# Kernel tuning notes

Measured on AMD Instinct MI355X. Metric: run time of the kernel, lower is better.

Reference implementation:

```python
import jax, jax.numpy as jnp
import numpy as np

NDIM = 2
NSIG = 2
NCELLS = 1000
BATCH = 4
DT = 1e-3
NSTEPS = 251  # 1 + int((t1 - t0)/dt) with t0=0, t1=0.25
SIGMA = 1e-3


def _phi(y, pw1, pb1, pw2, pb2, pw3, pb3, pw4, pb4, pw5, pb5):
    # phi_nn: 2 -> 16 -> 32 -> 32 -> 16 -> 1 with tanh activations
    h = jnp.tanh(y @ pw1.T + pb1)
    h = jnp.tanh(h @ pw2.T + pb2)
    h = jnp.tanh(h @ pw3.T + pb3)
    h = jnp.tanh(h @ pw4.T + pb4)
    return h @ pw5.T + pb5  # (ncells, 1)


def setup_inputs() -> dict:
    key = jax.random.key(0)
    ks = jax.random.split(key, 16)
    # x = [t0, t1, y0.flat, tcrit, p0(2), p1(2)] per batch item
    y0 = 0.1 * jax.random.normal(ks[0], (BATCH, NCELLS, NDIM), dtype=jnp.float32)
    t0 = jnp.zeros((BATCH, 1), jnp.float32)
    t1 = jnp.full((BATCH, 1), 0.25, jnp.float32)
    tcrit = jnp.full((BATCH, 1), 0.125, jnp.float32)
    p0 = jax.random.normal(ks[1], (BATCH, 2), dtype=jnp.float32)
    p1 = jax.random.normal(ks[2], (BATCH, 2), dtype=jnp.float32)
    x = jnp.concatenate([t0, t1, y0.reshape(BATCH, -1), tcrit, p0, p1], axis=1)
    # Wiener increments ~ N(0, dt)
    dw = np.sqrt(DT).astype(np.float32) * jax.random.normal(
        ks[3], (BATCH, NSTEPS, NCELLS, NDIM), dtype=jnp.float32)
    # phi_nn weights (torch Linear: weight is (out, in)), init N(0, 0.1), bias 0
    def w(k, o, i):
        return 0.1 * jax.random.normal(k, (o, i), dtype=jnp.float32)
    inp = dict(x=x, dw=dw,
               pw1=w(ks[4], 16, 2), pb1=jnp.zeros(16, jnp.float32),
               pw2=w(ks[5], 32, 16), pb2=jnp.zeros(32, jnp.float32),
               pw3=w(ks[6], 32, 32), pb3=jnp.zeros(32, jnp.float32),
               pw4=w(ks[7], 16, 32), pb4=jnp.zeros(16, jnp.float32),
               pw5=w(ks[8], 1, 16), pb5=jnp.zeros(1, jnp.float32),
               tw=w(ks[9], NDIM, NSIG), tb=jnp.zeros(NDIM, jnp.float32))
    return inp


def reference(x, dw, pw1, pb1, pw2, pb2, pw3, pb3, pw4, pb4, pw5, pb5, tw, tb):
    phi_params = (pw1, pb1, pw2, pb2, pw3, pb3, pw4, pb4, pw5, pb5)
    grad_phi = jax.grad(lambda yy: jnp.sum(_phi(yy, *phi_params)))

    def simulate(xi, dwi):
        t0 = xi[0]
        y0 = xi[2:2 + NCELLS * NDIM].reshape(NCELLS, NDIM)
        ps = xi[2 + NCELLS * NDIM:]
        tcrit, p0, p1 = ps[0], ps[1:3], ps[3:5]
        ts = t0 + DT * jnp.arange(NSTEPS, dtype=xi.dtype)

        def step(y, t_dw):
            t, dwt = t_dw
            sig = jnp.where(t < tcrit, p0, p1)      # step signal f_signal(t, params)
            tilt = sig @ tw.T + tb                  # grad_tilt: (ndim,)
            drift = -(grad_phi(y) + tilt)           # f(t, y)
            y_new = y + drift * DT + SIGMA * dwt    # Euler-Maruyama
            return y_new, None

        y_final, _ = jax.lax.scan(step, y0, (ts, dwi))
        return y_final

    return jax.vmap(simulate)(x, dw)  # (BATCH, NCELLS, NDIM)
```

## Files before the change

### kernel.cpp

```cpp
#include <hip/hip_runtime.h>

#define NDIMC 2
#define NCELLS 1000
#define BATCHSZ 4
#define NSTEPS 251
#define XROW 2007

typedef float v2f __attribute__((ext_vector_type(2)));
typedef float v4f __attribute__((ext_vector_type(4)));

__device__ __forceinline__ v2f vlo(v4f v) { return __builtin_shufflevector(v, v, 0, 1); }
__device__ __forceinline__ v2f vhi(v4f v) { return __builtin_shufflevector(v, v, 2, 3); }

__device__ __forceinline__ v2f pfma(v2f w, v2f v, v2f a) {
    return __builtin_elementwise_fma(w, v, a);
}

__device__ __forceinline__ float fast_tanh(float x) {
    float e = __builtin_amdgcn_exp2f(x * 2.885390081777926774f);
    float r = __builtin_amdgcn_rcpf(e + 1.0f);
    return fmaf(-2.0f, r, 1.0f);
}


template<int CTRL>
__device__ __forceinline__ float dpp_add(float z) {
    int t = __builtin_amdgcn_update_dpp(0, __float_as_int(z), CTRL, 0xf, 0xf, true);
    return z + __int_as_float(t);
}
__device__ __forceinline__ float row16_sum(float z) {
    z = dpp_add<0xB1>(z);
    z = dpp_add<0x1B>(z);
    z = dpp_add<0x141>(z);
    z = dpp_add<0x140>(z);
    return z;
}

__device__ __forceinline__ float pdot16(const v2f (&w)[8], const float* p, float bias) {
    v4f u0 = *(const v4f*)(p);
    v4f u1 = *(const v4f*)(p + 4);
    v4f u2 = *(const v4f*)(p + 8);
    v4f u3 = *(const v4f*)(p + 12);
    v2f a0 = {bias, 0.f}, a1 = {0.f, 0.f}, a2 = {0.f, 0.f}, a3 = {0.f, 0.f};
    a0 = pfma(w[0], vlo(u0), a0); a1 = pfma(w[1], vhi(u0), a1);
    a2 = pfma(w[2], vlo(u1), a2); a3 = pfma(w[3], vhi(u1), a3);
    a0 = pfma(w[4], vlo(u2), a0); a1 = pfma(w[5], vhi(u2), a1);
    a2 = pfma(w[6], vlo(u3), a2); a3 = pfma(w[7], vhi(u3), a3);
    v2f s = (a0 + a1) + (a2 + a3);
    return s[0] + s[1];
}

__device__ __forceinline__ float pdot32(const v2f (&w)[16], const float* p, float bias) {
    v2f a0 = {bias, 0.f}, a1 = {0.f, 0.f}, a2 = {0.f, 0.f}, a3 = {0.f, 0.f};
    #pragma unroll
    for (int c = 0; c < 2; ++c) {
        v4f u0 = *(const v4f*)(p + c * 16);
        v4f u1 = *(const v4f*)(p + c * 16 + 4);
        v4f u2 = *(const v4f*)(p + c * 16 + 8);
        v4f u3 = *(const v4f*)(p + c * 16 + 12);
        a0 = pfma(w[c*8+0], vlo(u0), a0); a1 = pfma(w[c*8+1], vhi(u0), a1);
        a2 = pfma(w[c*8+2], vlo(u1), a2); a3 = pfma(w[c*8+3], vhi(u1), a3);
        a0 = pfma(w[c*8+4], vlo(u2), a0); a1 = pfma(w[c*8+5], vhi(u2), a1);
        a2 = pfma(w[c*8+6], vlo(u3), a2); a3 = pfma(w[c*8+7], vhi(u3), a3);
    }
    v2f s = (a0 + a1) + (a2 + a3);
    return s[0] + s[1];
}

__global__ __launch_bounds__(64, 2)
void phinn_sde_kernel(const float* __restrict__ x,   const float* __restrict__ dw,
                      const float* __restrict__ pw1, const float* __restrict__ pb1,
                      const float* __restrict__ pw2, const float* __restrict__ pb2,
                      const float* __restrict__ pw3, const float* __restrict__ pb3,
                      const float* __restrict__ pw4, const float* __restrict__ pb4,
                      const float* __restrict__ pw5, const float* __restrict__ pb5,
                      const float* __restrict__ tw,  const float* __restrict__ tb,
                      float* __restrict__ out)
{
    __shared__ float sh[2][6][32];

    const int tid  = threadIdx.x;
    const int n    = tid & 31;
    const int grp  = tid >> 5;
    const int s16  = n & 15;
    const int b    = blockIdx.x / (NCELLS / 2);
    const int pair = blockIdx.x % (NCELLS / 2);
    const int cell = pair * 2 + grp;

    const float r1a = pw1[s16 * 2 + 0];
    const float r1b = pw1[s16 * 2 + 1];
    const float rb1 = pb1[s16];
    const float rb2 = pb2[n];
    const float rb3 = pb3[n];
    const float rb4 = pb4[s16];
    const float rw5 = pw5[s16];

    v2f w2p[8];
    #pragma unroll
    for (int j = 0; j < 8; ++j) w2p[j] = ((const v2f*)pw2)[n * 8 + j];

    v2f w3p[16];
    #pragma unroll
    for (int j = 0; j < 16; ++j) w3p[j] = ((const v2f*)pw3)[n * 16 + j];

    v2f w4p[16];
    #pragma unroll
    for (int j = 0; j < 16; ++j) w4p[j] = ((const v2f*)pw4)[s16 * 16 + j];

    v2f w4cp[8];
    #pragma unroll
    for (int j = 0; j < 8; ++j)
        w4cp[j] = v2f{pw4[(2*j) * 32 + n], pw4[(2*j+1) * 32 + n]};

    v2f w3cp[16];
    #pragma unroll
    for (int j = 0; j < 16; ++j)
        w3cp[j] = v2f{pw3[(2*j) * 32 + n], pw3[(2*j+1) * 32 + n]};

    v2f w2cp[16];
    #pragma unroll
    for (int j = 0; j < 16; ++j)
        w2cp[j] = v2f{pw2[(2*j) * 16 + s16], pw2[(2*j+1) * 16 + s16]};

    const float* xb = x + (size_t)b * XROW;
    const float t0v    = xb[0];
    const float tcritv = xb[2 + NCELLS * NDIMC];
    const float p0x = xb[2003], p0y = xb[2004];
    const float p1x = xb[2005], p1y = xb[2006];
    const float tA0 = fmaf(p0x, tw[0], fmaf(p0y, tw[1], tb[0]));
    const float tA1 = fmaf(p0x, tw[2], fmaf(p0y, tw[3], tb[1]));
    const float tB0 = fmaf(p1x, tw[0], fmaf(p1y, tw[1], tb[0]));
    const float tB1 = fmaf(p1x, tw[2], fmaf(p1y, tw[3], tb[1]));

    float y0 = xb[2 + cell * 2 + 0];
    float y1 = xb[2 + cell * 2 + 1];

    const float* dwb = dw + (size_t)b * NSTEPS * NCELLS * NDIMC
                          + (size_t)pair * 2 * NDIMC;
    int dwoff = grp * NDIMC;

    const float* l0 = &sh[grp][0][0];
    const float* l1 = &sh[grp][1][0];
    const float* l2 = &sh[grp][2][0];
    const float* l3 = &sh[grp][3][0];
    const float* l4 = &sh[grp][4][0];
    const float* l5 = &sh[grp][5][0];

    #pragma unroll 1
    for (int i = 0; i < NSTEPS; ++i) {
        const float2 dwv = *(const float2*)(dwb + dwoff);
        dwoff += NCELLS * NDIMC;
        const float t = t0v + 0.001f * (float)i;

        const float h1 = fast_tanh(fmaf(r1a, y0, fmaf(r1b, y1, rb1)));
        sh[grp][0][n] = h1;

        const float h2 = fast_tanh(pdot16(w2p, l0, rb2));
        sh[grp][1][n] = h2;

        const float h3 = fast_tanh(pdot32(w3p, l1, rb3));
        sh[grp][2][n] = h3;

        const float h4 = fast_tanh(pdot32(w4p, l2, rb4));

        const float g4p = rw5 * fmaf(-h4, h4, 1.0f);
        sh[grp][3][n] = g4p;

        const float g3p = pdot16(w4cp, l3, 0.f) * fmaf(-h3, h3, 1.0f);
        sh[grp][4][n] = g3p;

        const float g2p = pdot32(w3cp, l4, 0.f) * fmaf(-h2, h2, 1.0f);
        sh[grp][5][n] = g2p;

        const float g1p = pdot32(w2cp, l5, 0.f) * fmaf(-h1, h1, 1.0f);

        const float v0 = row16_sum(r1a * g1p);
        const float v1 = row16_sum(r1b * g1p);

        const bool  cnd   = t < tcritv;
        const float tilt0 = cnd ? tA0 : tB0;
        const float tilt1 = cnd ? tA1 : tB1;
        y0 = fmaf(-0.001f, v0 + tilt0, fmaf(0.001f, dwv.x, y0));
        y1 = fmaf(-0.001f, v1 + tilt1, fmaf(0.001f, dwv.y, y1));
    }

    if (n == 0) {
        *(float2*)(out + ((size_t)b * NCELLS + cell) * NDIMC) = make_float2(y0, y1);
    }
}

extern "C" void kernel_launch(void* const* d_in, const int* in_sizes, int n_in,
                              void* d_out, int out_size, void* d_ws, size_t ws_size,
                              hipStream_t stream) {
    const float* x   = (const float*)d_in[0];
    const float* dw  = (const float*)d_in[1];
    const float* pw1 = (const float*)d_in[2];
    const float* pb1 = (const float*)d_in[3];
    const float* pw2 = (const float*)d_in[4];
    const float* pb2 = (const float*)d_in[5];
    const float* pw3 = (const float*)d_in[6];
    const float* pb3 = (const float*)d_in[7];
    const float* pw4 = (const float*)d_in[8];
    const float* pb4 = (const float*)d_in[9];
    const float* pw5 = (const float*)d_in[10];
    const float* pb5 = (const float*)d_in[11];
    const float* tw  = (const float*)d_in[12];
    const float* tb  = (const float*)d_in[13];
    float* out = (float*)d_out;

    dim3 grid(BATCHSZ * NCELLS / 2);
    dim3 block(64);
    phinn_sde_kernel<<<grid, block, 0, stream>>>(x, dw, pw1, pb1, pw2, pb2,
                                                 pw3, pb3, pw4, pb4, pw5, pb5,
                                                 tw, tb, out);
}
```

Measured before the change: 271.4 us.

## Split each cell's dot products across two wave halves with permlane16 swap reduction

Each 64-thread block now handles one cell instead of two. The two 16-lane halves of each 32-lane group each compute half of every dot product, and the partial sums are combined with v_permlane16_swap. This halves the per-thread weight registers and the serial FMA chain length per step, and doubles the grid with a higher occupancy target in the launch bounds. The cost is twice as many wavefronts, an extra cross-lane swap per layer, and more redundant LDS traffic.

```diff
diff --git a/kernel.cpp b/kernel.cpp
--- a/kernel.cpp
+++ b/kernel.cpp
@@ -36,12 +36,28 @@
     return z;
 }
 
-__device__ __forceinline__ float pdot16(const v2f (&w)[8], const float* p, float bias) {
+__device__ __forceinline__ float xor16(float z, bool odd) {
+    float t = z, u = z;
+    asm("v_permlane16_swap_b32 %0, %1" : "+v"(t), "+v"(u));
+    return odd ? t : u;
+}
+
+__device__ __forceinline__ float pdot8h(const v2f (&w)[4], const float* p) {
+    v4f u0 = *(const v4f*)(p);
+    v4f u1 = *(const v4f*)(p + 4);
+    v2f a0 = {0.f, 0.f}, a1 = {0.f, 0.f};
+    a0 = pfma(w[0], vlo(u0), a0); a1 = pfma(w[1], vhi(u0), a1);
+    a0 = pfma(w[2], vlo(u1), a0); a1 = pfma(w[3], vhi(u1), a1);
+    v2f s = a0 + a1;
+    return s[0] + s[1];
+}
+
+__device__ __forceinline__ float pdot16h(const v2f (&w)[8], const float* p) {
     v4f u0 = *(const v4f*)(p);
     v4f u1 = *(const v4f*)(p + 4);
     v4f u2 = *(const v4f*)(p + 8);
     v4f u3 = *(const v4f*)(p + 12);
-    v2f a0 = {bias, 0.f}, a1 = {0.f, 0.f}, a2 = {0.f, 0.f}, a3 = {0.f, 0.f};
+    v2f a0 = {0.f, 0.f}, a1 = {0.f, 0.f}, a2 = {0.f, 0.f}, a3 = {0.f, 0.f};
     a0 = pfma(w[0], vlo(u0), a0); a1 = pfma(w[1], vhi(u0), a1);
     a2 = pfma(w[2], vlo(u1), a2); a3 = pfma(w[3], vhi(u1), a3);
     a0 = pfma(w[4], vlo(u2), a0); a1 = pfma(w[5], vhi(u2), a1);
@@ -50,24 +66,7 @@
     return s[0] + s[1];
 }
 
-__device__ __forceinline__ float pdot32(const v2f (&w)[16], const float* p, float bias) {
-    v2f a0 = {bias, 0.f}, a1 = {0.f, 0.f}, a2 = {0.f, 0.f}, a3 = {0.f, 0.f};
-    #pragma unroll
-    for (int c = 0; c < 2; ++c) {
-        v4f u0 = *(const v4f*)(p + c * 16);
-        v4f u1 = *(const v4f*)(p + c * 16 + 4);
-        v4f u2 = *(const v4f*)(p + c * 16 + 8);
-        v4f u3 = *(const v4f*)(p + c * 16 + 12);
-        a0 = pfma(w[c*8+0], vlo(u0), a0); a1 = pfma(w[c*8+1], vhi(u0), a1);
-        a2 = pfma(w[c*8+2], vlo(u1), a2); a3 = pfma(w[c*8+3], vhi(u1), a3);
-        a0 = pfma(w[c*8+4], vlo(u2), a0); a1 = pfma(w[c*8+5], vhi(u2), a1);
-        a2 = pfma(w[c*8+6], vlo(u3), a2); a3 = pfma(w[c*8+7], vhi(u3), a3);
-    }
-    v2f s = (a0 + a1) + (a2 + a3);
-    return s[0] + s[1];
-}
-
-__global__ __launch_bounds__(64, 2)
+__global__ __launch_bounds__(64, 4)
 void phinn_sde_kernel(const float* __restrict__ x,   const float* __restrict__ dw,
                       const float* __restrict__ pw1, const float* __restrict__ pb1,
                       const float* __restrict__ pw2, const float* __restrict__ pb2,
@@ -77,15 +76,16 @@
                       const float* __restrict__ tw,  const float* __restrict__ tb,
                       float* __restrict__ out)
 {
-    __shared__ float sh[2][6][32];
+    __shared__ float sh[6][32];
 
     const int tid  = threadIdx.x;
-    const int n    = tid & 31;
-    const int grp  = tid >> 5;
-    const int s16  = n & 15;
-    const int b    = blockIdx.x / (NCELLS / 2);
-    const int pair = blockIdx.x % (NCELLS / 2);
-    const int cell = pair * 2 + grp;
+    const int s16  = tid & 15;
+    const int r    = tid >> 4;
+    const int kh   = r & 1;
+    const bool odd = kh;
+    const int n    = s16 + ((r >> 1) << 4);
+    const int b    = blockIdx.x / NCELLS;
+    const int cell = blockIdx.x % NCELLS;
 
     const float r1a = pw1[s16 * 2 + 0];
     const float r1b = pw1[s16 * 2 + 1];
@@ -95,32 +95,32 @@
     const float rb4 = pb4[s16];
     const float rw5 = pw5[s16];
 
-    v2f w2p[8];
-    #pragma unroll
-    for (int j = 0; j < 8; ++j) w2p[j] = ((const v2f*)pw2)[n * 8 + j];
-
-    v2f w3p[16];
-    #pragma unroll
-    for (int j = 0; j < 16; ++j) w3p[j] = ((const v2f*)pw3)[n * 16 + j];
-
-    v2f w4p[16];
-    #pragma unroll
-    for (int j = 0; j < 16; ++j) w4p[j] = ((const v2f*)pw4)[s16 * 16 + j];
-
-    v2f w4cp[8];
+    v2f w2p[4];
+    #pragma unroll
+    for (int j = 0; j < 4; ++j) w2p[j] = ((const v2f*)pw2)[n * 8 + kh * 4 + j];
+
+    v2f w3p[8];
+    #pragma unroll
+    for (int j = 0; j < 8; ++j) w3p[j] = ((const v2f*)pw3)[n * 16 + kh * 8 + j];
+
+    v2f w4p[8];
+    #pragma unroll
+    for (int j = 0; j < 8; ++j) w4p[j] = ((const v2f*)pw4)[s16 * 16 + kh * 8 + j];
+
+    v2f w4cp[4];
+    #pragma unroll
+    for (int j = 0; j < 4; ++j)
+        w4cp[j] = v2f{pw4[(kh*8 + 2*j) * 32 + n], pw4[(kh*8 + 2*j + 1) * 32 + n]};
+
+    v2f w3cp[8];
     #pragma unroll
     for (int j = 0; j < 8; ++j)
-        w4cp[j] = v2f{pw4[(2*j) * 32 + n], pw4[(2*j+1) * 32 + n]};
-
-    v2f w3cp[16];
-    #pragma unroll
-    for (int j = 0; j < 16; ++j)
-        w3cp[j] = v2f{pw3[(2*j) * 32 + n], pw3[(2*j+1) * 32 + n]};
-
-    v2f w2cp[16];
-    #pragma unroll
-    for (int j = 0; j < 16; ++j)
-        w2cp[j] = v2f{pw2[(2*j) * 16 + s16], pw2[(2*j+1) * 16 + s16]};
+        w3cp[j] = v2f{pw3[(kh*16 + 2*j) * 32 + n], pw3[(kh*16 + 2*j + 1) * 32 + n]};
+
+    v2f w2cp[8];
+    #pragma unroll
+    for (int j = 0; j < 8; ++j)
+        w2cp[j] = v2f{pw2[(kh*16 + 2*j) * 16 + s16], pw2[(kh*16 + 2*j + 1) * 16 + s16]};
 
     const float* xb = x + (size_t)b * XROW;
     const float t0v    = xb[0];
@@ -135,47 +135,51 @@
     float y0 = xb[2 + cell * 2 + 0];
     float y1 = xb[2 + cell * 2 + 1];
 
-    const float* dwb = dw + (size_t)b * NSTEPS * NCELLS * NDIMC
-                          + (size_t)pair * 2 * NDIMC;
-    int dwoff = grp * NDIMC;
-
-    const float* l0 = &sh[grp][0][0];
-    const float* l1 = &sh[grp][1][0];
-    const float* l2 = &sh[grp][2][0];
-    const float* l3 = &sh[grp][3][0];
-    const float* l4 = &sh[grp][4][0];
-    const float* l5 = &sh[grp][5][0];
+    const float* dwp = dw + ((size_t)b * NSTEPS * NCELLS + cell) * NDIMC;
+
+    const float* l0 = &sh[0][0];
+    const float* l1 = &sh[1][0];
+    const float* l2 = &sh[2][0];
+    const float* l3 = &sh[3][0];
+    const float* l4 = &sh[4][0];
+    const float* l5 = &sh[5][0];
 
     #pragma unroll 1
     for (int i = 0; i < NSTEPS; ++i) {
-        const float2 dwv = *(const float2*)(dwb + dwoff);
-        dwoff += NCELLS * NDIMC;
+        const float2 dwv = *(const float2*)dwp;
+        dwp += NCELLS * NDIMC;
         const float t = t0v + 0.001f * (float)i;
 
         const float h1 = fast_tanh(fmaf(r1a, y0, fmaf(r1b, y1, rb1)));
-        sh[grp][0][n] = h1;
-
-        const float h2 = fast_tanh(pdot16(w2p, l0, rb2));
-        sh[grp][1][n] = h2;
-
-        const float h3 = fast_tanh(pdot32(w3p, l1, rb3));
-        sh[grp][2][n] = h3;
-
-        const float h4 = fast_tanh(pdot32(w4p, l2, rb4));
-
-        const float g4p = rw5 * fmaf(-h4, h4, 1.0f);
-        sh[grp][3][n] = g4p;
-
-        const float g3p = pdot16(w4cp, l3, 0.f) * fmaf(-h3, h3, 1.0f);
-        sh[grp][4][n] = g3p;
-
-        const float g2p = pdot32(w3cp, l4, 0.f) * fmaf(-h2, h2, 1.0f);
-        sh[grp][5][n] = g2p;
-
-        const float g1p = pdot32(w2cp, l5, 0.f) * fmaf(-h1, h1, 1.0f);
-
-        const float v0 = row16_sum(r1a * g1p);
-        const float v1 = row16_sum(r1b * g1p);
+        sh[0][s16] = h1;
+
+        const float p2 = pdot8h(w2p, l0 + kh * 8);
+        const float h2 = fast_tanh(p2 + xor16(p2, odd) + rb2);
+        sh[1][n] = h2;
+
+        const float p3 = pdot16h(w3p, l1 + kh * 16);
+        const float h3 = fast_tanh(p3 + xor16(p3, odd) + rb3);
+        sh[2][n] = h3;
+
+        const float p4 = pdot16h(w4p, l2 + kh * 16);
+        const float h4 = fast_tanh(p4 + xor16(p4, odd) + rb4);
+
+        const float g4 = rw5 * fmaf(-h4, h4, 1.0f);
+        sh[3][s16] = g4;
+
+        const float q3 = pdot8h(w4cp, l3 + kh * 8);
+        const float g3 = (q3 + xor16(q3, odd)) * fmaf(-h3, h3, 1.0f);
+        sh[4][n] = g3;
+
+        const float q2 = pdot16h(w3cp, l4 + kh * 16);
+        const float g2 = (q2 + xor16(q2, odd)) * fmaf(-h2, h2, 1.0f);
+        sh[5][n] = g2;
+
+        const float q1 = pdot16h(w2cp, l5 + kh * 16);
+        const float g1 = (q1 + xor16(q1, odd)) * fmaf(-h1, h1, 1.0f);
+
+        const float v0 = row16_sum(r1a * g1);
+        const float v1 = row16_sum(r1b * g1);
 
         const bool  cnd   = t < tcritv;
         const float tilt0 = cnd ? tA0 : tB0;
@@ -184,7 +188,7 @@
         y1 = fmaf(-0.001f, v1 + tilt1, fmaf(0.001f, dwv.y, y1));
     }
 
-    if (n == 0) {
+    if (tid == 0) {
         *(float2*)(out + ((size_t)b * NCELLS + cell) * NDIMC) = make_float2(y0, y1);
     }
 }
@@ -208,7 +212,7 @@
     const float* tb  = (const float*)d_in[13];
     float* out = (float*)d_out;
 
-    dim3 grid(BATCHSZ * NCELLS / 2);
+    dim3 grid(BATCHSZ * NCELLS);
     dim3 block(64);
     phinn_sde_kernel<<<grid, block, 0, stream>>>(x, dw, pw1, pb1, pw2, pb2,
                                                  pw3, pb3, pw4, pb4, pw5, pb5,
```

Result: slower. 346.3 us (+27.6%).

## Replace reverse-mode gradient with forward-mode tangent propagation through the MLP

Applied to the files above, without the earlier changes.

Instead of a forward pass followed by a backward pass with transposed weights, the kernel now propagates two tangent vectors (one per input dimension) alongside activations in a single forward sweep. Each layer's dot products run three times on the same weights, and the transposed weight registers are dropped. This cuts the serial chain of layer stages and shared-memory round trips from seven to four, and frees registers. In exchange each layer does three times the dot-product work, which adds arithmetic and LDS reads per step.

```diff
diff --git a/kernel.cpp b/kernel.cpp
--- a/kernel.cpp
+++ b/kernel.cpp
@@ -77,7 +77,7 @@
                       const float* __restrict__ tw,  const float* __restrict__ tb,
                       float* __restrict__ out)
 {
-    __shared__ float sh[2][6][32];
+    __shared__ __align__(16) float sh[2][3][3][32];
 
     const int tid  = threadIdx.x;
     const int n    = tid & 31;
@@ -106,21 +106,6 @@
     v2f w4p[16];
     #pragma unroll
     for (int j = 0; j < 16; ++j) w4p[j] = ((const v2f*)pw4)[s16 * 16 + j];
-
-    v2f w4cp[8];
-    #pragma unroll
-    for (int j = 0; j < 8; ++j)
-        w4cp[j] = v2f{pw4[(2*j) * 32 + n], pw4[(2*j+1) * 32 + n]};
-
-    v2f w3cp[16];
-    #pragma unroll
-    for (int j = 0; j < 16; ++j)
-        w3cp[j] = v2f{pw3[(2*j) * 32 + n], pw3[(2*j+1) * 32 + n]};
-
-    v2f w2cp[16];
-    #pragma unroll
-    for (int j = 0; j < 16; ++j)
-        w2cp[j] = v2f{pw2[(2*j) * 16 + s16], pw2[(2*j+1) * 16 + s16]};
 
     const float* xb = x + (size_t)b * XROW;
     const float t0v    = xb[0];
@@ -139,12 +124,15 @@
                           + (size_t)pair * 2 * NDIMC;
     int dwoff = grp * NDIMC;
 
-    const float* l0 = &sh[grp][0][0];
-    const float* l1 = &sh[grp][1][0];
-    const float* l2 = &sh[grp][2][0];
-    const float* l3 = &sh[grp][3][0];
-    const float* l4 = &sh[grp][4][0];
-    const float* l5 = &sh[grp][5][0];
+    const float* L0h = &sh[grp][0][0][0];
+    const float* L0a = &sh[grp][0][1][0];
+    const float* L0b = &sh[grp][0][2][0];
+    const float* L1h = &sh[grp][1][0][0];
+    const float* L1a = &sh[grp][1][1][0];
+    const float* L1b = &sh[grp][1][2][0];
+    const float* L2h = &sh[grp][2][0][0];
+    const float* L2a = &sh[grp][2][1][0];
+    const float* L2b = &sh[grp][2][2][0];
 
     #pragma unroll 1
     for (int i = 0; i < NSTEPS; ++i) {
@@ -153,29 +141,37 @@
         const float t = t0v + 0.001f * (float)i;
 
         const float h1 = fast_tanh(fmaf(r1a, y0, fmaf(r1b, y1, rb1)));
-        sh[grp][0][n] = h1;
-
-        const float h2 = fast_tanh(pdot16(w2p, l0, rb2));
-        sh[grp][1][n] = h2;
-
-        const float h3 = fast_tanh(pdot32(w3p, l1, rb3));
-        sh[grp][2][n] = h3;
-
-        const float h4 = fast_tanh(pdot32(w4p, l2, rb4));
-
-        const float g4p = rw5 * fmaf(-h4, h4, 1.0f);
-        sh[grp][3][n] = g4p;
-
-        const float g3p = pdot16(w4cp, l3, 0.f) * fmaf(-h3, h3, 1.0f);
-        sh[grp][4][n] = g3p;
-
-        const float g2p = pdot32(w3cp, l4, 0.f) * fmaf(-h2, h2, 1.0f);
-        sh[grp][5][n] = g2p;
-
-        const float g1p = pdot32(w2cp, l5, 0.f) * fmaf(-h1, h1, 1.0f);
-
-        const float v0 = row16_sum(r1a * g1p);
-        const float v1 = row16_sum(r1b * g1p);
+        const float d1 = fmaf(-h1, h1, 1.0f);
+        sh[grp][0][0][n] = h1;
+        sh[grp][0][1][n] = d1 * r1a;
+        sh[grp][0][2][n] = d1 * r1b;
+
+        const float a2 = pdot16(w2p, L0h, rb2);
+        const float q0 = pdot16(w2p, L0a, 0.f);
+        const float q1 = pdot16(w2p, L0b, 0.f);
+        const float h2 = fast_tanh(a2);
+        const float d2 = fmaf(-h2, h2, 1.0f);
+        sh[grp][1][0][n] = h2;
+        sh[grp][1][1][n] = d2 * q0;
+        sh[grp][1][2][n] = d2 * q1;
+
+        const float a3 = pdot32(w3p, L1h, rb3);
+        const float r0 = pdot32(w3p, L1a, 0.f);
+        const float r1 = pdot32(w3p, L1b, 0.f);
+        const float h3 = fast_tanh(a3);
+        const float d3 = fmaf(-h3, h3, 1.0f);
+        sh[grp][2][0][n] = h3;
+        sh[grp][2][1][n] = d3 * r0;
+        sh[grp][2][2][n] = d3 * r1;
+
+        const float a4 = pdot32(w4p, L2h, rb4);
+        const float s0 = pdot32(w4p, L2a, 0.f);
+        const float s1 = pdot32(w4p, L2b, 0.f);
+        const float h4 = fast_tanh(a4);
+        const float d4 = fmaf(-h4, h4, 1.0f);
+
+        const float v0 = row16_sum(rw5 * (d4 * s0));
+        const float v1 = row16_sum(rw5 * (d4 * s1));
 
         const bool  cnd   = t < tcritv;
         const float tilt0 = cnd ? tA0 : tB0;
```

New measurement: 328.8 us. +21.1%, slower.
